# Kernel tuning notes

Measured on AMD Instinct MI355X. Metric: run time of the kernel, lower is better.

## Reference

```python
import jax, jax.numpy as jnp
import numpy as np

A, Q, D, V = 64, 32, 180, 128  # n_queries, query_len, doc_len, embed_dim
B = 2 * A                      # in-batch passages (pos + neg)


def setup_inputs() -> dict:
    key = jax.random.key(0)
    kq, kp = jax.random.split(key)
    q = jax.random.normal(kq, (A, Q, V), dtype=jnp.float32)
    p = jax.random.normal(kp, (B, D, V), dtype=jnp.float32)
    return {"q": q, "p": p}


def reference(q, p):
    # in_batch_score (multi representation, cosine/dot interaction):
    # full query-passage interaction tensor [a, b, q, d]
    term_relevance = jnp.einsum('aqv,bdv->abqd', q, p)
    # term_relevance_to_final: maxsim over doc tokens, sum over query tokens
    query_maxsim = jnp.max(term_relevance, axis=-1)   # [a, b, q]
    relevance = jnp.sum(query_maxsim, axis=-1)        # [a, b]
    return term_relevance, query_maxsim, relevance
```

## Files before the change

### kernel.cpp

```cpp
#include <hip/hip_runtime.h>
#include <hip/hip_bf16.h>

#define A_N 64
#define B_N 128
#define Q_N 32
#define D_N 180
#define V_N 128

typedef __attribute__((ext_vector_type(8))) short bf16x8;
typedef __attribute__((ext_vector_type(4))) float f32x4;

__device__ __forceinline__ short f2bf(float f) {
  __hip_bfloat16 h = __float2bfloat16(f);
  return (short)__builtin_bit_cast(unsigned short, h);
}

__device__ __forceinline__ bf16x8 pack8(const f32x4& lo, const f32x4& hi) {
  bf16x8 v;
  v[0] = f2bf(lo[0]); v[1] = f2bf(lo[1]); v[2] = f2bf(lo[2]); v[3] = f2bf(lo[3]);
  v[4] = f2bf(hi[0]); v[5] = f2bf(hi[1]); v[6] = f2bf(hi[2]); v[7] = f2bf(hi[3]);
  return v;
}

__device__ __forceinline__ void lds_fence() {
  asm volatile("s_waitcnt lgkmcnt(0)" ::: "memory");
  __builtin_amdgcn_sched_barrier(0);
}

__global__ __launch_bounds__(512, 2) void score_kernel(
    const float* __restrict__ q, const float* __restrict__ p,
    float* __restrict__ out) {
  const int bid  = blockIdx.x;
  const int b    = bid & (B_N - 1);
  const int ag   = bid >> 7;
  const int tid  = threadIdx.x;
  const int wv   = tid >> 6;
  const int lane = tid & 63;
  const int l16  = lane & 15;
  const int g    = lane >> 4;

  const float* __restrict__ pb = p + (size_t)b * D_N * V_N;

  __shared__ ushort plds[D_N * V_N];
  __shared__ __align__(16) float cbuf[8][16 * D_N];
  for (int c = tid; c < D_N * (V_N / 8); c += 512) {
    const int r  = c >> 4;
    const int s  = c & 15;
    const int sp = (s & 8) | ((s & 7) ^ (r & 7));
    const float* src = pb + (size_t)r * V_N + s * 8;
    *reinterpret_cast<bf16x8*>(&plds[r * V_N + sp * 8]) =
        pack8(*reinterpret_cast<const f32x4*>(src),
              *reinterpret_cast<const f32x4*>(src + 4));
  }

  bf16x8 qf[2][2][4];
#define LOADQF(buf, jj)                                                       \
  {                                                                           \
    const int aq = ag * 32 + (jj) * 8 + wv;                                   \
    const float* __restrict__ qa = q + (size_t)aq * Q_N * V_N;                \
    _Pragma("unroll")                                                         \
    for (int qt = 0; qt < 2; ++qt)                                            \
      _Pragma("unroll")                                                       \
      for (int kk = 0; kk < 4; ++kk) {                                        \
        const float* s = qa + (size_t)(qt * 16 + l16) * V_N + kk * 32 + g * 8;\
        qf[buf][qt][kk] = pack8(*reinterpret_cast<const f32x4*>(s),          \
                                *reinterpret_cast<const f32x4*>(s + 4));     \
      }                                                                       \
  }
  LOADQF(0, 0);

  __syncthreads();

  float* cw = cbuf[wv];
  const size_t TERM_SZ = (size_t)A_N * B_N * Q_N * D_N;
  const size_t MS_SZ   = (size_t)A_N * B_N * Q_N;

#pragma unroll
  for (int j = 0; j < 4; ++j) {
    const int a  = ag * 32 + j * 8 + wv;
    const int jb = j & 1;

    f32x4 acc[2][12];
#pragma unroll
    for (int qt = 0; qt < 2; ++qt)
#pragma unroll
      for (int dt = 0; dt < 12; ++dt)
        acc[qt][dt] = (f32x4){0.f, 0.f, 0.f, 0.f};

#pragma unroll
    for (int dt = 0; dt < 12; ++dt) {
      const int drow = dt * 16 + l16;
      const int dr   = drow < D_N ? drow : (D_N - 1);

      bf16x8 pf[4];
#pragma unroll
      for (int kk = 0; kk < 4; ++kk) {
        const int s  = kk * 4 + g;
        const int sp = (s & 8) | ((s & 7) ^ (dr & 7));
        pf[kk] = *reinterpret_cast<const bf16x8*>(&plds[dr * V_N + sp * 8]);
      }
#pragma unroll
      for (int kk = 0; kk < 4; ++kk) {
        acc[0][dt] = __builtin_amdgcn_mfma_f32_16x16x32_bf16(pf[kk], qf[jb][0][kk], acc[0][dt], 0, 0, 0);
        acc[1][dt] = __builtin_amdgcn_mfma_f32_16x16x32_bf16(pf[kk], qf[jb][1][kk], acc[1][dt], 0, 0, 0);
      }
    }

    if (j < 3) LOADQF(!jb ? 1 : 0, j + 1);

    float qm[2] = {-INFINITY, -INFINITY};
#pragma unroll
    for (int qt = 0; qt < 2; ++qt)
#pragma unroll
      for (int dt = 0; dt < 12; ++dt)
        qm[qt] = fmaxf(qm[qt], fmaxf(fmaxf(acc[qt][dt][0], acc[qt][dt][1]),
                                     fmaxf(acc[qt][dt][2], acc[qt][dt][3])));

    const size_t outb = ((size_t)a * B_N + b) * (size_t)(Q_N * D_N);
#pragma unroll
    for (int qt = 0; qt < 2; ++qt) {
#pragma unroll
      for (int dt = 0; dt < 12; ++dt) {
        if (dt < 11 || g == 0)
          *reinterpret_cast<f32x4*>(&cw[l16 * D_N + dt * 16 + g * 4]) = acc[qt][dt];
      }
      lds_fence();

#pragma unroll
      for (int c = 0; c < 12; ++c) {
        const int off = c * 256 + lane * 4;
        if (c < 11 || lane < 16) {
          f32x4 v = *reinterpret_cast<const f32x4*>(&cw[off]);
          *reinterpret_cast<f32x4*>(out + outb + (size_t)qt * 16 * D_N + off) = v;
        }
      }
      lds_fence();
    }

    float qm0 = qm[0], qm1 = qm[1];
    qm0 = fmaxf(qm0, __shfl_xor(qm0, 16, 64));
    qm0 = fmaxf(qm0, __shfl_xor(qm0, 32, 64));
    qm1 = fmaxf(qm1, __shfl_xor(qm1, 16, 64));
    qm1 = fmaxf(qm1, __shfl_xor(qm1, 32, 64));

    if (lane < 16) {
      float* ms = out + TERM_SZ + ((size_t)a * B_N + b) * Q_N;
      ms[lane]      = qm0;
      ms[16 + lane] = qm1;
    }

    float s = qm0 + qm1;
    s += __shfl_xor(s, 1, 64);
    s += __shfl_xor(s, 2, 64);
    s += __shfl_xor(s, 4, 64);
    s += __shfl_xor(s, 8, 64);
    if (lane == 0)
      out[TERM_SZ + MS_SZ + (size_t)a * B_N + b] = s;
  }
#undef LOADQF
}

extern "C" void kernel_launch(void* const* d_in, const int* in_sizes, int n_in,
                              void* d_out, int out_size, void* d_ws, size_t ws_size,
                              hipStream_t stream) {
  const float* q = (const float*)d_in[0];
  const float* p = (const float*)d_in[1];
  float* out = (float*)d_out;
  dim3 grid(256);
  dim3 block(512);
  hipLaunchKernelGGL(score_kernel, grid, block, 0, stream, q, p, out);
}
```

Before: 43.00 us.

## Overlap second-half tile global stores with next iteration's MFMA loop

The second q-tile of each iteration is now left staged in LDS, and its copy to global memory is interleaved with the MFMA loop of the following iteration, one chunk per d-tile. A final epilogue flushes the last tile. The aim is to hide global store traffic behind matrix compute, so the output write does not serialise after the compute. In exchange the store and LDS read instructions are mixed into the MFMA stream, and the layout of the LDS buffer has to stay consistent from one iteration to the next.

```diff
diff --git a/kernel.cpp b/kernel.cpp
--- a/kernel.cpp
+++ b/kernel.cpp
@@ -79,6 +79,10 @@
   for (int j = 0; j < 4; ++j) {
     const int a  = ag * 32 + j * 8 + wv;
     const int jb = j & 1;
+    const size_t outb_prev = (j > 0)
+        ? ((size_t)(ag * 32 + (j - 1) * 8 + wv) * B_N + b) * (size_t)(Q_N * D_N)
+          + (size_t)16 * D_N
+        : 0;
 
     f32x4 acc[2][12];
 #pragma unroll
@@ -104,7 +108,16 @@
         acc[0][dt] = __builtin_amdgcn_mfma_f32_16x16x32_bf16(pf[kk], qf[jb][0][kk], acc[0][dt], 0, 0, 0);
         acc[1][dt] = __builtin_amdgcn_mfma_f32_16x16x32_bf16(pf[kk], qf[jb][1][kk], acc[1][dt], 0, 0, 0);
       }
-    }
+
+      if (j > 0) {
+        const int off = dt * 256 + lane * 4;
+        if (dt < 11 || lane < 16) {
+          f32x4 v = *reinterpret_cast<const f32x4*>(&cw[off]);
+          *reinterpret_cast<f32x4*>(out + outb_prev + off) = v;
+        }
+      }
+    }
+    if (j > 0) lds_fence();
 
     if (j < 3) LOADQF(!jb ? 1 : 0, j + 1);
 
@@ -117,25 +130,29 @@
                                      fmaxf(acc[qt][dt][2], acc[qt][dt][3])));
 
     const size_t outb = ((size_t)a * B_N + b) * (size_t)(Q_N * D_N);
-#pragma unroll
-    for (int qt = 0; qt < 2; ++qt) {
-#pragma unroll
-      for (int dt = 0; dt < 12; ++dt) {
-        if (dt < 11 || g == 0)
-          *reinterpret_cast<f32x4*>(&cw[l16 * D_N + dt * 16 + g * 4]) = acc[qt][dt];
-      }
-      lds_fence();
-
-#pragma unroll
-      for (int c = 0; c < 12; ++c) {
-        const int off = c * 256 + lane * 4;
-        if (c < 11 || lane < 16) {
-          f32x4 v = *reinterpret_cast<const f32x4*>(&cw[off]);
-          *reinterpret_cast<f32x4*>(out + outb + (size_t)qt * 16 * D_N + off) = v;
-        }
-      }
-      lds_fence();
-    }
+
+#pragma unroll
+    for (int dt = 0; dt < 12; ++dt) {
+      if (dt < 11 || g == 0)
+        *reinterpret_cast<f32x4*>(&cw[l16 * D_N + dt * 16 + g * 4]) = acc[0][dt];
+    }
+    lds_fence();
+#pragma unroll
+    for (int c = 0; c < 12; ++c) {
+      const int off = c * 256 + lane * 4;
+      if (c < 11 || lane < 16) {
+        f32x4 v = *reinterpret_cast<const f32x4*>(&cw[off]);
+        *reinterpret_cast<f32x4*>(out + outb + off) = v;
+      }
+    }
+    lds_fence();
+
+#pragma unroll
+    for (int dt = 0; dt < 12; ++dt) {
+      if (dt < 11 || g == 0)
+        *reinterpret_cast<f32x4*>(&cw[l16 * D_N + dt * 16 + g * 4]) = acc[1][dt];
+    }
+    lds_fence();
 
     float qm0 = qm[0], qm1 = qm[1];
     qm0 = fmaxf(qm0, __shfl_xor(qm0, 16, 64));
@@ -158,6 +175,20 @@
       out[TERM_SZ + MS_SZ + (size_t)a * B_N + b] = s;
   }
 #undef LOADQF
+
+  {
+    const int a3 = ag * 32 + 3 * 8 + wv;
+    const size_t outb3 = ((size_t)a3 * B_N + b) * (size_t)(Q_N * D_N)
+                         + (size_t)16 * D_N;
+#pragma unroll
+    for (int c = 0; c < 12; ++c) {
+      const int off = c * 256 + lane * 4;
+      if (c < 11 || lane < 16) {
+        f32x4 v = *reinterpret_cast<const f32x4*>(&cw[off]);
+        *reinterpret_cast<f32x4*>(out + outb3 + off) = v;
+      }
+    }
+  }
 }
 
 extern "C" void kernel_launch(void* const* d_in, const int* in_sizes, int n_in,
```

After: 44.12 us. 2.6% more time.
